# Kernel tuning notes

Measured on AMD Instinct MI355X. Metric: run time of the kernel, lower is better.

## Reference

```python
import jax, jax.numpy as jnp
import numpy as np

DIM = 768
H = 6        # pinned by router mask construction (3 logits -> 6 head gates)
HD = DIM // H  # 128
TAU = 5.0

def setup_inputs() -> dict:
    key = jax.random.key(0)
    ks = jax.random.split(key, 10)
    w = 0.02
    return {
        "x": jax.random.normal(ks[0], (4, 2048, DIM), jnp.float32),
        "latency": jax.random.uniform(ks[1], (1,), jnp.float32),
        "qkv_w": jax.random.normal(ks[2], (3 * DIM, DIM), jnp.float32) * w,
        "qkv_b": jax.random.normal(ks[3], (3 * DIM,), jnp.float32) * w,
        "proj_w": jax.random.normal(ks[4], (DIM, DIM), jnp.float32) * w,
        "proj_b": jax.random.normal(ks[5], (DIM,), jnp.float32) * w,
        "router_w": jax.random.normal(ks[6], (3, 1), jnp.float32),
        "router_b": jax.random.normal(ks[7], (3,), jnp.float32),
        # gumbel noise g = -log(Exp(1)), matching -empty.exponential_().log()
        "g1": -jnp.log(jax.random.exponential(ks[8], (3,), jnp.float32)),
        "g2": -jnp.log(jax.random.exponential(ks[9], (3,), jnp.float32)),
    }

def reference(x, latency, qkv_w, qkv_b, proj_w, proj_b, router_w, router_b, g1, g2):
    # router: Linear(1, 3) on scalar latency -> 3 logits
    logits = router_w @ latency + router_b                      # [3]
    # gumbel-sigmoid, tau=5, hard=True with straight-through estimator
    y_soft = jax.nn.sigmoid((logits + g1 - g2) / TAU)           # [3]
    y_hard = (y_soft > 0.5).astype(y_soft.dtype)
    mask3 = y_hard - jax.lax.stop_gradient(y_soft) + y_soft     # [3]
    # first logit gates 4 heads, remaining two gate one head each -> 6 heads
    mask6 = jnp.concatenate([mask3[:1], mask3[:1], mask3[:1], mask3])  # [6]
    maskC = jnp.repeat(mask6, HD)                               # [DIM]

    B, N, C = x.shape
    qkv = jnp.einsum('bnc,oc->bno', x, qkv_w) + qkv_b           # [B,N,3*DIM]
    qkv = qkv.reshape(B, N, 3, H, HD)
    q, k, v = qkv[:, :, 0], qkv[:, :, 1], qkv[:, :, 2]          # [B,N,H,HD]

    scale = HD ** -0.5
    attn = jax.nn.softmax(jnp.einsum('bqhd,bkhd->bhqk', q * scale, k), axis=-1)
    out = jnp.einsum('bhqk,bkhd->bqhd', attn, v).reshape(B, N, C)

    out = out * maskC                                            # gate heads/channels
    return jnp.einsum('bnc,oc->bno', out, proj_w) + proj_b
```

## Files before the change

### kernel.cpp

```cpp
#include <hip/hip_runtime.h>
#include <cstdint>

#define DIM_ 768
#define H_ 6
#define HD_ 128
#define NB_ 4
#define SEQ_ 2048
#define TOK_ (NB_*SEQ_)
#define OUT3_ (3*DIM_)
#define L2E 1.4426950408889634f

typedef __bf16 bf16;
typedef __bf16 bf16x4 __attribute__((ext_vector_type(4)));
typedef __bf16 bf16x8 __attribute__((ext_vector_type(8)));
typedef float f32x4 __attribute__((ext_vector_type(4)));
typedef float f32x16 __attribute__((ext_vector_type(16)));
typedef unsigned int u32;
typedef u32 u32x4 __attribute__((ext_vector_type(4)));

__device__ __forceinline__ void gload16(const void* g, void* lds) {
  __builtin_amdgcn_global_load_lds((const __attribute__((address_space(1))) void*)g,
                                   (__attribute__((address_space(3))) void*)lds,
                                   16, 0, 0);
}

__global__ void convert_kernel(const float* __restrict__ in, bf16* __restrict__ out, int n) {
  int i = (blockIdx.x * 256 + threadIdx.x) * 4;
  if (i >= n) return;
  float4 v = *reinterpret_cast<const float4*>(in + i);
  bf16x4 o = { (bf16)v.x, (bf16)v.y, (bf16)v.z, (bf16)v.w };
  *reinterpret_cast<bf16x4*>(out + i) = o;
}

__global__ void mask_kernel(const float* __restrict__ latency,
                            const float* __restrict__ rw,
                            const float* __restrict__ rb,
                            const float* __restrict__ g1,
                            const float* __restrict__ g2,
                            float* __restrict__ mask6) {
  int i = threadIdx.x;
  if (i < 6) {
    int j = (i < 4) ? 0 : (i - 3);
    float logit = rw[j] * latency[0] + rb[j];
    float z = (logit + g1[j] - g2[j]) / 5.0f;
    float ys = 1.0f / (1.0f + expf(-z));
    float yh = ys > 0.5f ? 1.0f : 0.0f;
    mask6[i] = (yh - ys) + ys;
  }
}


__global__ __launch_bounds__(256)
void qkv_gemm(const bf16* __restrict__ A, const bf16* __restrict__ W,
              const float* __restrict__ bias, const float* __restrict__ mask6,
              bf16* __restrict__ q, bf16* __restrict__ k, bf16* __restrict__ vt) {
  __shared__ bf16 SM[16384];
  bf16* As = SM;
  bf16* Bs = SM + 8192;
  bf16* Frag = SM;
  const int tid = threadIdx.x;
  const int l = tid & 63, w = tid >> 6;
  const int lr = l & 15, lg = l >> 4;
  const int wm = w >> 1, wn = w & 1;
  const int tm = blockIdx.y * 128;
  const int on = blockIdx.x * 128;

  const int sblk = (on < DIM_) ? 0 : (on < 2 * DIM_ ? 1 : 2);
  const int hblk = (on - sblk * DIM_) >> 7;
  if (mask6[hblk] == 0.0f) return;

  const int lrow = l >> 3;
  const int scol = ((l & 7) ^ lrow) * 8;

  f32x4 acc[4][4];
#pragma unroll
  for (int i = 0; i < 4; ++i)
#pragma unroll
    for (int j = 0; j < 4; ++j) acc[i][j] = f32x4{0.f, 0.f, 0.f, 0.f};

  for (int k0 = 0; k0 < DIM_; k0 += 64) {
    __syncthreads();
#pragma unroll
    for (int u = 0; u < 4; ++u) {
      int br = w * 32 + u * 8;
      gload16(A + (size_t)(tm + br + lrow) * DIM_ + k0 + scol, As + br * 64);
      gload16(W + (size_t)(on + br + lrow) * DIM_ + k0 + scol, Bs + br * 64);
    }
    __syncthreads();
#pragma unroll
    for (int kk = 0; kk < 2; ++kk) {
      bf16x8 af[4], bfr[4];
#pragma unroll
      for (int i = 0; i < 4; ++i) {
        int row = wm * 64 + i * 16 + lr;
        af[i] = *reinterpret_cast<const bf16x8*>(As + row * 64 + (((kk << 2) + lg) ^ (row & 7)) * 8);
      }
#pragma unroll
      for (int j = 0; j < 4; ++j) {
        int row = wn * 64 + j * 16 + lr;
        bfr[j] = *reinterpret_cast<const bf16x8*>(Bs + row * 64 + (((kk << 2) + lg) ^ (row & 7)) * 8);
      }
#pragma unroll
      for (int i = 0; i < 4; ++i)
#pragma unroll
        for (int j = 0; j < 4; ++j)
          acc[i][j] = __builtin_amdgcn_mfma_f32_16x16x32_bf16(af[i], bfr[j], acc[i][j], 0, 0, 0);
    }
  }

  const int n0 = tm & 2047;
  const int bb = tm >> 11;
  const int bhh = bb * H_ + hblk;

  if (on < 2 * DIM_) {
    const int s = sblk;
    const float scale = 0.08838834764831845f * L2E;
    bf16* dstbase = (s == 0) ? q : k;
    __syncthreads();
#pragma unroll
    for (int i = 0; i < 4; ++i) {
#pragma unroll
      for (int j = 0; j < 4; ++j) {
        int dd = wn * 64 + j * 16 + lr;
        int kc = dd >> 4, hi8 = (dd >> 3) & 1, e = dd & 7;
        float bia = bias[on + dd];
#pragma unroll
        for (int r = 0; r < 4; ++r) {
          int nl = wm * 64 + i * 16 + lg * 4 + r;
          float val = acc[i][j][r] + bia;
          if (s == 0) val *= scale;
          Frag[(((nl >> 5) * 8 + kc) << 9) + ((hi8 * 32 + (nl & 31)) << 3) + e] = (bf16)val;
        }
      }
    }
    __syncthreads();
    size_t base = ((size_t)bhh * 64 + (n0 >> 5)) * 4096;
#pragma unroll
    for (int it = 0; it < 8; ++it) {
      int idx = it * 2048 + tid * 8;
      bf16x8 v8 = *reinterpret_cast<const bf16x8*>(Frag + idx);
      *reinterpret_cast<bf16x8*>(dstbase + base + idx) = v8;
    }
  } else {
    bf16(*Ts)[136] = reinterpret_cast<bf16(*)[136]>(Frag);
    for (int wc = 0; wc < 2; ++wc) {
      __syncthreads();
      if (wn == wc) {
#pragma unroll
        for (int j = 0; j < 4; ++j) {
          float bia = bias[on + wc * 64 + j * 16 + lr];
#pragma unroll
          for (int i = 0; i < 4; ++i) {
            bf16x4 pk;
#pragma unroll
            for (int r = 0; r < 4; ++r) pk[r] = (bf16)(acc[i][j][r] + bia);
            *reinterpret_cast<bf16x4*>(&Ts[j * 16 + lr][wm * 64 + i * 16 + lg * 4]) = pk;
          }
        }
      }
      __syncthreads();
#pragma unroll
      for (int it = 0; it < 4; ++it) {
        int row = it * 16 + (tid >> 4);
        int c8 = (tid & 15) * 8;
        bf16x8 v8 = *reinterpret_cast<const bf16x8*>(&Ts[row][c8]);
        int d = wc * 64 + row;
        int n = n0 + c8;
        size_t idx = (((((size_t)bhh * 32 + (n >> 6)) * 4 + ((n >> 4) & 3)) * 4 + (d >> 5)) << 9) +
                     ((((n >> 3) & 1) * 32 + (d & 31)) << 3);
        *reinterpret_cast<bf16x8*>(vt + idx) = v8;
      }
    }
  }
}

__global__ __launch_bounds__(256)
void proj_gemm(const bf16* __restrict__ A, const bf16* __restrict__ W,
               const float* __restrict__ bias, const float* __restrict__ mask6,
               float* __restrict__ out) {
  __shared__ bf16 As[128 * 64];
  __shared__ bf16 Bs[64 * 64];
  const int tid = threadIdx.x;
  const int l = tid & 63, w = tid >> 6;
  const int lr = l & 15, lg = l >> 4;
  const int wm = w >> 1, wn = w & 1;
  const int tm = blockIdx.y * 128;
  const int on = blockIdx.x * 64;

  const int lrow = l >> 3;
  const int scol = ((l & 7) ^ lrow) * 8;

  f32x4 acc[4][2];
#pragma unroll
  for (int i = 0; i < 4; ++i)
#pragma unroll
    for (int j = 0; j < 2; ++j) acc[i][j] = f32x4{0.f, 0.f, 0.f, 0.f};

  for (int k0 = 0; k0 < DIM_; k0 += 64) {
    if (mask6[k0 >> 7] == 0.0f) continue;
    __syncthreads();
#pragma unroll
    for (int u = 0; u < 4; ++u) {
      int br = w * 32 + u * 8;
      gload16(A + (size_t)(tm + br + lrow) * DIM_ + k0 + scol, As + br * 64);
    }
#pragma unroll
    for (int u = 0; u < 2; ++u) {
      int br = w * 16 + u * 8;
      gload16(W + (size_t)(on + br + lrow) * DIM_ + k0 + scol, Bs + br * 64);
    }
    __syncthreads();
#pragma unroll
    for (int kk = 0; kk < 2; ++kk) {
      bf16x8 af[4], bfr[2];
#pragma unroll
      for (int i = 0; i < 4; ++i) {
        int row = wm * 64 + i * 16 + lr;
        af[i] = *reinterpret_cast<const bf16x8*>(As + row * 64 + (((kk << 2) + lg) ^ (row & 7)) * 8);
      }
#pragma unroll
      for (int j = 0; j < 2; ++j) {
        int row = wn * 32 + j * 16 + lr;
        bfr[j] = *reinterpret_cast<const bf16x8*>(Bs + row * 64 + (((kk << 2) + lg) ^ (row & 7)) * 8);
      }
#pragma unroll
      for (int i = 0; i < 4; ++i)
#pragma unroll
        for (int j = 0; j < 2; ++j)
          acc[i][j] = __builtin_amdgcn_mfma_f32_16x16x32_bf16(af[i], bfr[j], acc[i][j], 0, 0, 0);
    }
  }

#pragma unroll
  for (int i = 0; i < 4; ++i) {
#pragma unroll
    for (int j = 0; j < 2; ++j) {
      int o = on + wn * 32 + j * 16 + lr;
      float bia = bias[o];
#pragma unroll
      for (int r = 0; r < 4; ++r) {
        int t = tm + wm * 64 + i * 16 + lg * 4 + r;
        out[(size_t)t * DIM_ + o] = acc[i][j][r] + bia;
      }
    }
  }
}

__global__ __launch_bounds__(128, 2)
void attn_kernel(const bf16* __restrict__ qf_g, const bf16* __restrict__ kf_g,
                 const bf16* __restrict__ vf_g, const float* __restrict__ mask6,
                 bf16* __restrict__ ab) {
  __shared__ char smem[16640];

  const int tid = threadIdx.x;
  const int l = tid & 63;
  const int w = tid >> 6;
  const int kl = l & 31, hi = l >> 5;
  const int bid = blockIdx.x;
  const int bh = bid % 24;
  const int qt = bid / 24;
  const int h = bh % H_;
  const int b = bh / H_;
  const int q0 = qt * 32;
  const int loff = l * 8;
  const float hm = mask6[h];

  if (hm == 0.0f) {
    bf16x8 z = __builtin_bit_cast(bf16x8, u32x4{0u, 0u, 0u, 0u});
    int row = tid >> 2, c0 = (tid & 3) * 32;
    bf16* dst = ab + ((size_t)b * SEQ_ + q0 + row) * DIM_ + h * HD_ + c0;
#pragma unroll
    for (int u = 0; u < 4; ++u)
      *reinterpret_cast<bf16x8*>(dst + u * 8) = z;
    return;
  }

  float* OM  = (float*)smem;
  float* MLm = (float*)(smem + 16384);
  float* MLl = MLm + 32;

  const bf16* qq = qf_g + (((size_t)bh * 64 + qt) * 8) * 512;
  const bf16* kq = kf_g + (size_t)bh * 262144 + (size_t)w * 32 * 4096;
  const bf16* vq = vf_g + (size_t)bh * 262144 + (size_t)w * 32 * 4096;

  bf16x8 qf[8];
#pragma unroll
  for (int kc = 0; kc < 8; ++kc)
    qf[kc] = *reinterpret_cast<const bf16x8*>(qq + kc * 512 + loff);

  f32x16 oacc[4];
#pragma unroll
  for (int df = 0; df < 4; ++df)
#pragma unroll
    for (int r = 0; r < 16; ++r) oacc[df][r] = 0.f;
  float m_lane = -3.0e38f;
  float lsum = 0.f;

  for (int jj = 0; jj < 32; ++jj) {
    const bf16* kb = kq + (size_t)jj * 4096;
    const bf16* vb = vq + (size_t)jj * 4096;

    f32x16 sacc;
#pragma unroll
    for (int r = 0; r < 16; ++r) sacc[r] = 0.f;
    __builtin_amdgcn_s_setprio(1);
#pragma unroll
    for (int kc = 0; kc < 8; ++kc) {
      bf16x8 kfr = *reinterpret_cast<const bf16x8*>(kb + kc * 512 + loff);
      sacc = __builtin_amdgcn_mfma_f32_32x32x16_bf16(kfr, qf[kc], sacc, 0, 0, 0);
    }
    __builtin_amdgcn_s_setprio(0);

    float t = sacc[0];
#pragma unroll
    for (int r = 1; r < 16; ++r) t = fmaxf(t, sacc[r]);
    t = fmaxf(t, __shfl_xor(t, 32));
    bool need = t > m_lane + 8.0f;
    if (__ballot(need) != 0ull) {
      float nm = fmaxf(m_lane, t);
      float c = exp2f(m_lane - nm);
      m_lane = nm;
      lsum *= c;
#pragma unroll
      for (int r = 0; r < 16; ++r) {
        float cr = __shfl(c, (r & 3) + 8 * (r >> 2) + 4 * hi);
#pragma unroll
        for (int df = 0; df < 4; ++df) oacc[df][r] *= cr;
      }
    }

    u32 pp[8];
#pragma unroll
    for (int m = 0; m < 8; ++m) {
      float e0 = exp2f(sacc[2 * m] - m_lane);
      float e1 = exp2f(sacc[2 * m + 1] - m_lane);
      lsum += e0 + e1;
      union { u32 u; bf16 hh2[2]; } pk;
      pk.hh2[0] = (bf16)e0; pk.hh2[1] = (bf16)e1;
      pp[m] = pk.u;
    }

    u32x4 afv[2];
#pragma unroll
    for (int ks = 0; ks < 2; ++ks) {
#pragma unroll
      for (int i = 0; i < 2; ++i) {
        u32 a = pp[4 * ks + i];
        u32 b2 = pp[4 * ks + 2 + i];
        asm volatile("v_permlane32_swap_b32 %0, %1" : "+v"(a), "+v"(b2));
        afv[ks][i] = a;
        afv[ks][2 + i] = b2;
      }
    }

    __builtin_amdgcn_s_setprio(1);
#pragma unroll
    for (int ks = 0; ks < 2; ++ks) {
      bf16x8 pa = __builtin_bit_cast(bf16x8, afv[ks]);
#pragma unroll
      for (int df = 0; df < 4; ++df) {
        bf16x8 vfr = *reinterpret_cast<const bf16x8*>(vb + (ks * 4 + df) * 512 + loff);
        oacc[df] = __builtin_amdgcn_mfma_f32_32x32x16_bf16(pa, vfr, oacc[df], 0, 0, 0);
      }
    }
    __builtin_amdgcn_s_setprio(0);
  }

  float lt = lsum + __shfl_xor(lsum, 32);

  if (w == 1) {
#pragma unroll
    for (int r = 0; r < 16; ++r) {
      int qloc = (r & 3) + 8 * (r >> 2) + 4 * hi;
#pragma unroll
      for (int df = 0; df < 4; ++df)
        OM[qloc * 128 + df * 32 + kl] = oacc[df][r];
    }
    MLm[kl] = m_lane;
    MLl[kl] = lt;
  }
  __syncthreads();
  if (w == 1) return;

  float m1 = MLm[kl];
  float l1 = MLl[kl];
  float M = fmaxf(m_lane, m1);
  float a0 = exp2f(m_lane - M), a1 = exp2f(m1 - M);
  float L = lt * a0 + l1 * a1;
  float s0 = a0 * hm / L, s1 = a1 * hm / L;

#pragma unroll
  for (int r = 0; r < 16; ++r) {
    int qloc = (r & 3) + 8 * (r >> 2) + 4 * hi;
    float r0 = __shfl(s0, qloc);
    float r1 = __shfl(s1, qloc);
    int n = q0 + qloc;
#pragma unroll
    for (int df = 0; df < 4; ++df) {
      int d = df * 32 + kl;
      float o1 = OM[qloc * 128 + df * 32 + kl];
      ab[((size_t)b * SEQ_ + n) * DIM_ + h * HD_ + d] =
          (bf16)(oacc[df][r] * r0 + o1 * r1);
    }
  }
}

extern "C" void kernel_launch(void* const* d_in, const int* in_sizes, int n_in,
                              void* d_out, int out_size, void* d_ws, size_t ws_size,
                              hipStream_t stream) {
  const float* x        = (const float*)d_in[0];
  const float* latency  = (const float*)d_in[1];
  const float* qkv_w    = (const float*)d_in[2];
  const float* qkv_b    = (const float*)d_in[3];
  const float* proj_w   = (const float*)d_in[4];
  const float* proj_b   = (const float*)d_in[5];
  const float* router_w = (const float*)d_in[6];
  const float* router_b = (const float*)d_in[7];
  const float* g1       = (const float*)d_in[8];
  const float* g2       = (const float*)d_in[9];
  float* out = (float*)d_out;

  const size_t N_X  = (size_t)TOK_ * DIM_;
  const size_t N_WQ = (size_t)OUT3_ * DIM_;
  const size_t N_WP = (size_t)DIM_ * DIM_;
  const size_t N_P  = (size_t)NB_ * H_ * SEQ_ * HD_;

  float* maskp = (float*)d_ws;
  bf16* xb  = (bf16*)((char*)d_ws + 256);
  bf16* wqb = xb + N_X;
  bf16* wpb = wqb + N_WQ;
  bf16* qbf = wpb + N_WP;
  bf16* kbf = qbf + N_P;
  bf16* vtb = kbf + N_P;
  bf16* abf = vtb + N_P;

  size_t need = 256 + 2 * (N_X + N_WQ + N_WP + 4 * N_P);
  if (ws_size < need) return;

  mask_kernel<<<1, 64, 0, stream>>>(latency, router_w, router_b, g1, g2, maskp);
  convert_kernel<<<(int)(N_X / 1024), 256, 0, stream>>>(x, xb, (int)N_X);
  convert_kernel<<<(int)(N_WQ / 1024), 256, 0, stream>>>(qkv_w, wqb, (int)N_WQ);
  convert_kernel<<<(int)(N_WP / 1024), 256, 0, stream>>>(proj_w, wpb, (int)N_WP);

  qkv_gemm<<<dim3(OUT3_ / 128, TOK_ / 128), 256, 0, stream>>>(xb, wqb, qkv_b, maskp, qbf, kbf, vtb);
  attn_kernel<<<dim3(24 * (SEQ_ / 32)), 128, 0, stream>>>(qbf, kbf, vtb, maskp, abf);
  proj_gemm<<<dim3(DIM_ / 64, TOK_ / 128), 256, 0, stream>>>(abf, wpb, proj_b, maskp, out);
}
```

Baseline: 179.4 us.

## Double-buffer QKV and proj GEMM LDS tiles and fuse prep kernels into one

After: 171.5 us (median of 2 runs). 4.4% less time.

```diff
diff --git a/kernel.cpp b/kernel.cpp
--- a/kernel.cpp
+++ b/kernel.cpp
@@ -24,22 +24,15 @@
                                    16, 0, 0);
 }
 
-__global__ void convert_kernel(const float* __restrict__ in, bf16* __restrict__ out, int n) {
-  int i = (blockIdx.x * 256 + threadIdx.x) * 4;
-  if (i >= n) return;
-  float4 v = *reinterpret_cast<const float4*>(in + i);
-  bf16x4 o = { (bf16)v.x, (bf16)v.y, (bf16)v.z, (bf16)v.w };
-  *reinterpret_cast<bf16x4*>(out + i) = o;
-}
-
-__global__ void mask_kernel(const float* __restrict__ latency,
-                            const float* __restrict__ rw,
-                            const float* __restrict__ rb,
-                            const float* __restrict__ g1,
+__global__ void prep_kernel(const float* __restrict__ x, const float* __restrict__ qw,
+                            const float* __restrict__ pw,
+                            const float* __restrict__ latency, const float* __restrict__ rw,
+                            const float* __restrict__ rb, const float* __restrict__ g1,
                             const float* __restrict__ g2,
-                            float* __restrict__ mask6) {
-  int i = threadIdx.x;
-  if (i < 6) {
+                            bf16* __restrict__ xb, bf16* __restrict__ wqb,
+                            bf16* __restrict__ wpb, float* __restrict__ mask6) {
+  if (blockIdx.x == 0 && threadIdx.x < 6) {
+    int i = threadIdx.x;
     int j = (i < 4) ? 0 : (i - 3);
     float logit = rw[j] * latency[0] + rb[j];
     float z = (logit + g1[j] - g2[j]) / 5.0f;
@@ -47,6 +40,18 @@
     float yh = ys > 0.5f ? 1.0f : 0.0f;
     mask6[i] = (yh - ys) + ys;
   }
+  const int QX  = TOK_ * DIM_ / 4;
+  const int QWQ = OUT3_ * DIM_ / 4;
+  int gid = blockIdx.x * 256 + threadIdx.x;
+  const float* src;
+  bf16* dst;
+  int off;
+  if (gid < QX) { src = x; dst = xb; off = gid; }
+  else if (gid < QX + QWQ) { src = qw; dst = wqb; off = gid - QX; }
+  else { src = pw; dst = wpb; off = gid - QX - QWQ; }
+  float4 v = *reinterpret_cast<const float4*>(src + off * 4);
+  bf16x4 o = { (bf16)v.x, (bf16)v.y, (bf16)v.z, (bf16)v.w };
+  *reinterpret_cast<bf16x4*>(dst + off * 4) = o;
 }
 
 
@@ -54,10 +59,8 @@
 void qkv_gemm(const bf16* __restrict__ A, const bf16* __restrict__ W,
               const float* __restrict__ bias, const float* __restrict__ mask6,
               bf16* __restrict__ q, bf16* __restrict__ k, bf16* __restrict__ vt) {
-  __shared__ bf16 SM[16384];
-  bf16* As = SM;
-  bf16* Bs = SM + 8192;
-  bf16* Frag = SM;
+  __shared__ bf16 AB[2][8192];
+  bf16* Frag = &AB[0][0];
   const int tid = threadIdx.x;
   const int l = tid & 63, w = tid >> 6;
   const int lr = l & 15, lg = l >> 4;
@@ -69,8 +72,8 @@
   const int hblk = (on - sblk * DIM_) >> 7;
   if (mask6[hblk] == 0.0f) return;
 
-  const int lrow = l >> 3;
-  const int scol = ((l & 7) ^ lrow) * 8;
+  const int lrow = l >> 2;
+  const int scol = ((l & 3) ^ (lrow & 3)) * 8;
 
   f32x4 acc[4][4];
 #pragma unroll
@@ -78,34 +81,38 @@
 #pragma unroll
     for (int j = 0; j < 4; ++j) acc[i][j] = f32x4{0.f, 0.f, 0.f, 0.f};
 
-  for (int k0 = 0; k0 < DIM_; k0 += 64) {
+  auto STAGE = [&](int k0, int buf) {
+#pragma unroll
+    for (int u = 0; u < 2; ++u) {
+      int rbase = w * 32 + u * 16;
+      gload16(A + (size_t)(tm + rbase + lrow) * DIM_ + k0 + scol, &AB[buf][rbase * 32]);
+      gload16(W + (size_t)(on + rbase + lrow) * DIM_ + k0 + scol, &AB[buf][4096 + rbase * 32]);
+    }
+  };
+
+  STAGE(0, 0);
+  __syncthreads();
+  for (int t = 0; t < 24; ++t) {
+    if (t + 1 < 24) STAGE((t + 1) * 32, (t + 1) & 1);
+    const bf16* As = &AB[t & 1][0];
+    const bf16* Bs = &AB[t & 1][4096];
+    bf16x8 af[4], bfr[4];
+#pragma unroll
+    for (int i = 0; i < 4; ++i) {
+      int row = wm * 64 + i * 16 + lr;
+      af[i] = *reinterpret_cast<const bf16x8*>(As + row * 32 + ((lg ^ (row & 3)) * 8));
+    }
+#pragma unroll
+    for (int j = 0; j < 4; ++j) {
+      int row = wn * 64 + j * 16 + lr;
+      bfr[j] = *reinterpret_cast<const bf16x8*>(Bs + row * 32 + ((lg ^ (row & 3)) * 8));
+    }
+#pragma unroll
+    for (int i = 0; i < 4; ++i)
+#pragma unroll
+      for (int j = 0; j < 4; ++j)
+        acc[i][j] = __builtin_amdgcn_mfma_f32_16x16x32_bf16(af[i], bfr[j], acc[i][j], 0, 0, 0);
     __syncthreads();
-#pragma unroll
-    for (int u = 0; u < 4; ++u) {
-      int br = w * 32 + u * 8;
-      gload16(A + (size_t)(tm + br + lrow) * DIM_ + k0 + scol, As + br * 64);
-      gload16(W + (size_t)(on + br + lrow) * DIM_ + k0 + scol, Bs + br * 64);
-    }
-    __syncthreads();
-#pragma unroll
-    for (int kk = 0; kk < 2; ++kk) {
-      bf16x8 af[4], bfr[4];
-#pragma unroll
-      for (int i = 0; i < 4; ++i) {
-        int row = wm * 64 + i * 16 + lr;
-        af[i] = *reinterpret_cast<const bf16x8*>(As + row * 64 + (((kk << 2) + lg) ^ (row & 7)) * 8);
-      }
-#pragma unroll
-      for (int j = 0; j < 4; ++j) {
-        int row = wn * 64 + j * 16 + lr;
-        bfr[j] = *reinterpret_cast<const bf16x8*>(Bs + row * 64 + (((kk << 2) + lg) ^ (row & 7)) * 8);
-      }
-#pragma unroll
-      for (int i = 0; i < 4; ++i)
-#pragma unroll
-        for (int j = 0; j < 4; ++j)
-          acc[i][j] = __builtin_amdgcn_mfma_f32_16x16x32_bf16(af[i], bfr[j], acc[i][j], 0, 0, 0);
-    }
   }
 
   const int n0 = tm & 2047;
@@ -116,7 +123,6 @@
     const int s = sblk;
     const float scale = 0.08838834764831845f * L2E;
     bf16* dstbase = (s == 0) ? q : k;
-    __syncthreads();
 #pragma unroll
     for (int i = 0; i < 4; ++i) {
 #pragma unroll
@@ -176,10 +182,8 @@
 
 __global__ __launch_bounds__(256)
 void proj_gemm(const bf16* __restrict__ A, const bf16* __restrict__ W,
-               const float* __restrict__ bias, const float* __restrict__ mask6,
-               float* __restrict__ out) {
-  __shared__ bf16 As[128 * 64];
-  __shared__ bf16 Bs[64 * 64];
+               const float* __restrict__ bias, float* __restrict__ out) {
+  __shared__ bf16 AB[2][12288];
   const int tid = threadIdx.x;
   const int l = tid & 63, w = tid >> 6;
   const int lr = l & 15, lg = l >> 4;
@@ -196,20 +200,25 @@
 #pragma unroll
     for (int j = 0; j < 2; ++j) acc[i][j] = f32x4{0.f, 0.f, 0.f, 0.f};
 
-  for (int k0 = 0; k0 < DIM_; k0 += 64) {
-    if (mask6[k0 >> 7] == 0.0f) continue;
-    __syncthreads();
+  auto STAGE = [&](int k0, int buf) {
 #pragma unroll
     for (int u = 0; u < 4; ++u) {
       int br = w * 32 + u * 8;
-      gload16(A + (size_t)(tm + br + lrow) * DIM_ + k0 + scol, As + br * 64);
+      gload16(A + (size_t)(tm + br + lrow) * DIM_ + k0 + scol, &AB[buf][br * 64]);
     }
 #pragma unroll
     for (int u = 0; u < 2; ++u) {
       int br = w * 16 + u * 8;
-      gload16(W + (size_t)(on + br + lrow) * DIM_ + k0 + scol, Bs + br * 64);
-    }
-    __syncthreads();
+      gload16(W + (size_t)(on + br + lrow) * DIM_ + k0 + scol, &AB[buf][8192 + br * 64]);
+    }
+  };
+
+  STAGE(0, 0);
+  __syncthreads();
+  for (int t = 0; t < 12; ++t) {
+    if (t + 1 < 12) STAGE((t + 1) * 64, (t + 1) & 1);
+    const bf16* As = &AB[t & 1][0];
+    const bf16* Bs = &AB[t & 1][8192];
 #pragma unroll
     for (int kk = 0; kk < 2; ++kk) {
       bf16x8 af[4], bfr[2];
@@ -229,6 +238,7 @@
         for (int j = 0; j < 2; ++j)
           acc[i][j] = __builtin_amdgcn_mfma_f32_16x16x32_bf16(af[i], bfr[j], acc[i][j], 0, 0, 0);
     }
+    __syncthreads();
   }
 
 #pragma unroll
@@ -437,12 +447,11 @@
   size_t need = 256 + 2 * (N_X + N_WQ + N_WP + 4 * N_P);
   if (ws_size < need) return;
 
-  mask_kernel<<<1, 64, 0, stream>>>(latency, router_w, router_b, g1, g2, maskp);
-  convert_kernel<<<(int)(N_X / 1024), 256, 0, stream>>>(x, xb, (int)N_X);
-  convert_kernel<<<(int)(N_WQ / 1024), 256, 0, stream>>>(qkv_w, wqb, (int)N_WQ);
-  convert_kernel<<<(int)(N_WP / 1024), 256, 0, stream>>>(proj_w, wpb, (int)N_WP);
+  const int prep_blocks = (int)((N_X + N_WQ + N_WP) / 1024);
+  prep_kernel<<<prep_blocks, 256, 0, stream>>>(x, qkv_w, proj_w, latency, router_w,
+                                               router_b, g1, g2, xb, wqb, wpb, maskp);
 
   qkv_gemm<<<dim3(OUT3_ / 128, TOK_ / 128), 256, 0, stream>>>(xb, wqb, qkv_b, maskp, qbf, kbf, vtb);
   attn_kernel<<<dim3(24 * (SEQ_ / 32)), 128, 0, stream>>>(qbf, kbf, vtb, maskp, abf);
-  proj_gemm<<<dim3(DIM_ / 64, TOK_ / 128), 256, 0, stream>>>(abf, wpb, proj_b, maskp, out);
-}
+  proj_gemm<<<dim3(DIM_ / 64, TOK_ / 128), 256, 0, stream>>>(abf, wpb, proj_b, out);
+}
```
